# Optimization experiments

Measured on AMD Instinct MI355X. Metric: run time of the kernel, lower is better.

Reference implementation:

```python
import jax, jax.numpy as jnp
import numpy as np

R = 3
D = 2 * R + 1            # 7 displacements per axis
B, C, H, W = 2, 128, 48, 96
EPS = 1e-5


def conv2d(x, w, stride=1, padding=1):
    return jax.lax.conv_general_dilated(
        x, w, (stride, stride), [(padding, padding), (padding, padding)],
        dimension_numbers=('NCHW', 'OIHW', 'NCHW'))


def deconv2d(x, w, stride=2, padding=1):
    # w: torch ConvTranspose2d layout (I, O, kh, kw)
    wf = jnp.flip(w, (2, 3)).transpose(1, 0, 2, 3)  # -> OIHW, spatially flipped
    p = w.shape[2] - 1 - padding
    return jax.lax.conv_general_dilated(
        x, wf, (1, 1), [(p, p), (p, p)], lhs_dilation=(stride, stride),
        dimension_numbers=('NCHW', 'OIHW', 'NCHW'))


def bn_relu(x, g, b):
    # BatchNorm2d, training-mode statistics (biased variance), then ReLU
    mu = x.mean(axis=(0, 2, 3), keepdims=True)
    var = x.var(axis=(0, 2, 3), keepdims=True)
    xn = (x - mu) * jax.lax.rsqrt(var + EPS)
    return jax.nn.relu(xn * g[None, :, None, None] + b[None, :, None, None])


def grid_sample_zeros(img, gx, gy):
    # img: (B,C,H,W); gx, gy: (B,S) pixel coords. Bilinear, zero padding,
    # align_corners=True (coords already in pixel space -> identity unnormalize).
    b, c, h, w = img.shape
    x0 = jnp.floor(gx)
    y0 = jnp.floor(gy)
    wx = gx - x0
    wy = gy - y0
    imgf = img.reshape(b, c, h * w)

    def corner(xi, yi, wgt):
        valid = (xi >= 0) & (xi < w) & (yi >= 0) & (yi < h)
        xi_c = jnp.clip(xi, 0, w - 1).astype(jnp.int32)
        yi_c = jnp.clip(yi, 0, h - 1).astype(jnp.int32)
        lin = (yi_c * w + xi_c)[:, None, :]            # (B,1,S)
        v = jnp.take_along_axis(imgf, lin, axis=2)     # (B,C,S)
        return v * (wgt * valid)[:, None, :]

    return (corner(x0, y0, (1 - wx) * (1 - wy))
            + corner(x0 + 1, y0, wx * (1 - wy))
            + corner(x0, y0 + 1, (1 - wx) * wy)
            + corner(x0 + 1, y0 + 1, wx * wy))


def setup_inputs() -> dict:
    key = jax.random.key(0)
    ks = jax.random.split(key, 24)
    s = 0.05
    f1 = jax.random.normal(ks[0], (B, C, H, W), dtype=jnp.float32)
    f2 = jax.random.normal(ks[1], (B, C, H, W), dtype=jnp.float32)
    cx = jax.random.uniform(ks[2], (B, 1, H, W), dtype=jnp.float32) * (W - 1)
    cy = jax.random.uniform(ks[3], (B, 1, H, W), dtype=jnp.float32) * (H - 1)
    coords = jnp.concatenate([cx, cy], axis=1)  # (B,2,H,W): [x, y]
    p = {
        'w1': jax.random.normal(ks[4], (96, 2 * C, 3, 3)) * s,
        'g1': jnp.ones((96,)), 'b1': jnp.zeros((96,)),
        'w2': jax.random.normal(ks[5], (128, 96, 3, 3)) * s,
        'g2': jnp.ones((128,)), 'b2': jnp.zeros((128,)),
        'w3': jax.random.normal(ks[6], (128, 128, 3, 3)) * s,
        'g3': jnp.ones((128,)), 'b3': jnp.zeros((128,)),
        'w4': jax.random.normal(ks[7], (64, 128, 3, 3)) * s,
        'g4': jnp.ones((64,)), 'b4': jnp.zeros((64,)),
        'w5': jax.random.normal(ks[8], (64, 32, 4, 4)) * s,  # ConvTranspose (I,O,kh,kw)
        'g5': jnp.ones((32,)), 'b5': jnp.zeros((32,)),
        'w6': jax.random.normal(ks[9], (1, 32, 3, 3)) * s,
        'b6': jnp.zeros((1,)),
        'dap_w': jnp.eye(D * D, dtype=jnp.float32),  # identity init
    }
    return {'f1': f1, 'f2': f2, 'coords': coords, **p}


def reference(f1, f2, coords, w1, g1, b1, w2, g2, b2, w3, g3, b3,
              w4, g4, b4, w5, g5, b5, w6, b6, dap_w):
    b, c, h, w = f1.shape
    dx = jnp.linspace(-R, R, D)
    delta = jnp.stack(jnp.meshgrid(dx, dx, indexing='ij'), axis=-1)  # (D,D,2)
    cen = (coords.transpose(0, 2, 3, 1).reshape(b, 1, h, 1, w, 2)
           + delta.reshape(1, D, 1, D, 1, 2))                        # (B,D,H,D,W,2)
    gx = cen[..., 0].reshape(b, -1)
    gy = cen[..., 1].reshape(b, -1)
    f2s = grid_sample_zeros(f2, gx, gy).reshape(b, c, D, h, D, w)
    f2s = f2s.transpose(0, 2, 4, 1, 3, 5)                            # (B,D,D,C,H,W)
    f1e = jnp.broadcast_to(f1[:, None, None], (b, D, D, c, h, w))
    corr = jnp.concatenate([f1e, f2s], axis=3).reshape(b * D * D, 2 * c, h, w)
    x = bn_relu(conv2d(corr, w1), g1, b1)
    x = bn_relu(conv2d(x, w2, stride=2), g2, b2)
    x = bn_relu(conv2d(x, w3), g3, b3)
    x = bn_relu(conv2d(x, w4), g4, b4)
    x = bn_relu(deconv2d(x, w5), g5, b5)
    x = conv2d(x, w6) + b6[None, :, None, None]
    cost = x.reshape(b, D * D, h, w)
    cost = jnp.einsum('ed,bdhw->behw', dap_w, cost)  # DAP 1x1 conv, no bias
    return cost  # (B, (2r+1)^2, H, W)
```

## Files before the change

### kernel.cpp

```cpp
#include <hip/hip_runtime.h>
#include <hip/hip_bf16.h>

using bf16 = __hip_bfloat16;
typedef __attribute__((ext_vector_type(8))) short s8v;
typedef __attribute__((ext_vector_type(4))) float f4v;
typedef __attribute__((ext_vector_type(16))) float f16v;

static constexpr int Bb = 2, Hh = 48, Ww = 96;
static constexpr int HW = Hh * Ww;
static constexpr int DD = 49, Nn = Bb * DD;
static constexpr int H2 = 24, W2 = 48, HW2 = H2 * W2;

static constexpr size_t off_wf1a = 0;
static constexpr size_t off_wf1b = 221184;
static constexpr size_t off_wf3  = 442368;
static constexpr size_t off_wf2  = 737280;
static constexpr size_t off_wf4  = 958464;
static constexpr size_t off_wf5  = 1105920;
static constexpr size_t off_f1t  = 1171456;
static constexpr size_t off_y1a  = 3530752;
static constexpr size_t off_stats= 7069696;
static constexpr size_t off_f2s  = 7079936;
static constexpr size_t off_y1   = 122685440;
static constexpr size_t off_f2t  = off_y1;
static constexpr size_t off_y2   = off_f2s;
static constexpr size_t off_y3   = off_f2s + 28901376;
static constexpr size_t off_y4   = off_f2s + 57802752;
static constexpr size_t off_y5   = off_f2s + 72253440;
static constexpr size_t off_y6   = off_f2s + 101154816;
static constexpr size_t WS_NEEDED = 209389568;

__device__ __forceinline__ float bf2f(unsigned short h) {
  return __uint_as_float(((unsigned)h) << 16);
}
__device__ __forceinline__ unsigned short f2bf(float f) {
  __hip_bfloat16 h = __float2bfloat16(f);
  union { __hip_bfloat16 x; unsigned short u; } cv; cv.x = h; return cv.u;
}
template<bool EN>
__device__ __forceinline__ uint4 bn8(uint4 v, const float* a, const float* b, int c0) {
  if constexpr (!EN) return v;
  union { uint4 u; unsigned short h[8]; } X; X.u = v;
#pragma unroll
  for (int i = 0; i < 8; ++i) {
    float f = fmaxf(bf2f(X.h[i]) * a[c0 + i] + b[c0 + i], 0.f);
    X.h[i] = f2bf(f);
  }
  return X.u;
}
__device__ __forceinline__ s8v as_s8v(uint4 v) {
  union { uint4 u; s8v s; } cv; cv.u = v; return cv.s;
}

__global__ __launch_bounds__(256) void zero_k(float* __restrict__ p, int n) {
  int i = blockIdx.x * 256 + threadIdx.x;
  if (i < n) p[i] = 0.f;
}

__global__ __launch_bounds__(256) void tr_f2_k(const float* __restrict__ f2, float* __restrict__ f2t) {
  int o = blockIdx.x * 256 + threadIdx.x;
  if (o >= 2 * HW * 16) return;
  int c8 = o & 15; int pos = (o >> 4) % HW; int b = o / (HW * 16);
  float v[8];
#pragma unroll
  for (int i = 0; i < 8; ++i) v[i] = f2[((size_t)(b * 128 + c8 * 8 + i)) * HW + pos];
  float* dst = f2t + ((size_t)b * HW + pos) * 128 + c8 * 8;
#pragma unroll
  for (int i = 0; i < 8; ++i) dst[i] = v[i];
}

__global__ __launch_bounds__(256) void tr_f1_k(const float* __restrict__ f1, bf16* __restrict__ f1t) {
  int o = blockIdx.x * 256 + threadIdx.x;
  if (o >= 2 * HW * 16) return;
  int c8 = o & 15; int pos = (o >> 4) % HW; int b = o / (HW * 16);
  union { uint4 u; unsigned short h[8]; } Y;
#pragma unroll
  for (int i = 0; i < 8; ++i) Y.h[i] = f2bf(f1[((size_t)(b * 128 + c8 * 8 + i)) * HW + pos]);
  *(uint4*)(f1t + ((size_t)b * HW + pos) * 128 + c8 * 8) = Y.u;
}

__global__ __launch_bounds__(256)
void prep32_k(const float* __restrict__ w, uint4* __restrict__ wf, int NT, int CINT, int ciOff) {
  int idx = blockIdx.x * 256 + threadIdx.x;
  int total = 9 * 2 * 4 * NT * 64;
  if (idx >= total) return;
  int ocl = idx & 31; int lh = (idx >> 5) & 1;
  int q = idx >> 6; int nt = q % NT; int rest = q / NT;
  int ks = rest & 3; int cih = (rest >> 2) & 1; int khw = rest >> 3;
  int oc = nt * 32 + ocl;
  union { uint4 u; unsigned short h[8]; } Y;
#pragma unroll
  for (int i = 0; i < 8; ++i) {
    int ci = ciOff + cih * 64 + ks * 16 + lh * 8 + i;
    Y.h[i] = f2bf(w[((size_t)oc * CINT + ci) * 9 + khw]);
  }
  wf[idx] = Y.u;
}

__global__ __launch_bounds__(256)
void prep16_k(const float* __restrict__ w, uint4* __restrict__ wf, int NT, int CINT,
              int NSTAGE, int CPS, int KPS) {
  int idx = blockIdx.x * 256 + threadIdx.x;
  int total = 9 * NSTAGE * KPS * NT * 64;
  if (idx >= total) return;
  int ocl = idx & 15; int lg = (idx >> 4) & 3;
  int q = idx >> 6; int nt = q % NT; int q2 = q / NT;
  int ks = q2 % KPS; int q3 = q2 / KPS;
  int st = q3 % NSTAGE; int khw = q3 / NSTAGE;
  int oc = nt * 16 + ocl;
  union { uint4 u; unsigned short h[8]; } Y;
#pragma unroll
  for (int i = 0; i < 8; ++i) {
    int ci = st * CPS + ks * 32 + lg * 8 + i;
    Y.h[i] = f2bf(w[((size_t)oc * CINT + ci) * 9 + khw]);
  }
  wf[idx] = Y.u;
}

__global__ __launch_bounds__(256)
void prep_w5_k(const float* __restrict__ w5, uint4* __restrict__ wf) {
  int idx = blockIdx.x * 256 + threadIdx.x;
  if (idx >= 4096) return;
  int ocl = idx & 15; int lg = (idx >> 4) & 3;
  int nt = (idx >> 6) & 1; int ks = (idx >> 7) & 7; int p = idx >> 10;
  int ph = p >> 1, pw = p & 1;
  int t = ks >> 2, u = (ks >> 1) & 1;
  int kh = 3 - ph - 2 * t, kw = 3 - pw - 2 * u;
  int oc = nt * 16 + ocl;
  union { uint4 u4; unsigned short h[8]; } Y;
#pragma unroll
  for (int i = 0; i < 8; ++i) {
    int ci = (ks & 1) * 32 + lg * 8 + i;
    Y.h[i] = f2bf(w5[(((size_t)ci * 32 + oc) * 4 + kh) * 4 + kw]);
  }
  wf[idx] = Y.u4;
}

__global__ __launch_bounds__(256)
void sample_k(const float* __restrict__ f2t, const float* __restrict__ coords,
              bf16* __restrict__ f2s) {
  int wv = blockIdx.x * 4 + (threadIdx.x >> 6);
  int lane = threadIdx.x & 63;
  int p0 = wv * 32;
  for (int k = 0; k < 32; ++k) {
    int P = p0 + k;
    int hw = P % HW; int n = P / HW;
    int b = n / DD, d = n % DD;
    float gx = coords[(size_t)b * 2 * HW + hw] + (float)(d / 7 - 3);
    float gy = coords[((size_t)b * 2 + 1) * HW + hw] + (float)(d % 7 - 3);
    float x0f = floorf(gx), y0f = floorf(gy);
    float wx = gx - x0f, wy = gy - y0f;
    int x0 = (int)x0f, y0 = (int)y0f;
    const float* base = f2t + (size_t)b * HW * 128;
    float r0 = 0.f, r1 = 0.f;
#pragma unroll
    for (int c = 0; c < 4; ++c) {
      int xi = x0 + (c & 1), yi = y0 + (c >> 1);
      float wgt = ((c & 1) ? wx : 1.f - wx) * ((c >> 1) ? wy : 1.f - wy);
      if (xi < 0 || xi >= Ww || yi < 0 || yi >= Hh) wgt = 0.f;
      int xc = min(max(xi, 0), Ww - 1), yc = min(max(yi, 0), Hh - 1);
      const float* pv = base + ((size_t)(yc * Ww + xc)) * 128 + 2 * lane;
      r0 += wgt * pv[0];
      r1 += wgt * pv[1];
    }
    unsigned pack = (unsigned)f2bf(r0) | ((unsigned)f2bf(r1) << 16);
    ((unsigned*)f2s)[(size_t)P * 64 + lane] = pack;
  }
}

template<int COUT, int NT, int MT, int NB, int GR, int GC, bool OUTF32, bool HAS_BASE,
         bool HAS_BN, bool HAS_STATS>
__global__ __launch_bounds__(((GR * GC) / MT) * (NT / NB) * 64)
void conv32_k(const bf16* __restrict__ in, const uint4* __restrict__ wf,
              void* __restrict__ outv, const float* __restrict__ base,
              const float* __restrict__ bn_a, const float* __restrict__ bn_b,
              float* __restrict__ stats,
              int N, int H, int W, int DIV) {
  constexpr int NW = ((GR * GC) / MT) * (NT / NB);
  constexpr int BR = GR * 2, BC = GC * 16;
  constexpr int IR = BR + 2, IC = BC + 2;
  constexpr int INB = IR * IC * 128;
  __shared__ __align__(16) char lds[INB];

  const int tid = threadIdx.x;
  const int lane = tid & 63;
  const int wv = tid >> 6;
  const int lm = lane & 31, lh = lane >> 5;
  const int dh = lm >> 4, dw = lm & 15;
  constexpr int NG = NT / NB;
  const int mg = wv / NG, ng = wv % NG;

  const int tW = W / BC, tH = H / BR;
  const int tile = blockIdx.x % (tH * tW);
  const int n = blockIdx.x / (tH * tW);
  const int oh0 = (tile / tW) * BR, ow0 = (tile % tW) * BC;
  const size_t inbase = (size_t)n * H * W * 128;

  int trA[MT], tcA[MT];
#pragma unroll
  for (int i = 0; i < MT; ++i) { int mt = mg * MT + i; trA[i] = mt / GC; tcA[i] = mt % GC; }

  f16v acc[MT][NB];
#pragma unroll
  for (int i = 0; i < MT; ++i)
#pragma unroll
    for (int j = 0; j < NB; ++j)
#pragma unroll
      for (int r = 0; r < 16; ++r) acc[i][j][r] = 0.f;

  for (int cih = 0; cih < 2; ++cih) {
    __syncthreads();
    for (int idx = tid; idx < IR * IC * 8; idx += NW * 64) {
      int h8 = idx & 7;
      int icl = (idx >> 3) % IC;
      int ihl = (idx >> 3) / IC;
      int ih = oh0 - 1 + ihl, iw = ow0 - 1 + icl;
      uint4 v = make_uint4(0u, 0u, 0u, 0u);
      if (ih >= 0 && ih < H && iw >= 0 && iw < W) {
        v = *(const uint4*)(in + inbase + ((size_t)(ih * W + iw)) * 128 + cih * 64 + h8 * 8);
        v = bn8<HAS_BN>(v, bn_a, bn_b, cih * 64 + h8 * 8);
      }
      int bbyte = (ihl * IC + icl) * 128 + h8 * 16;
      bbyte ^= (icl & 7) << 4;
      *(uint4*)(lds + bbyte) = v;
    }
    __syncthreads();

    for (int khw = 0; khw < 9; ++khw) {
      const int kh = khw / 3, kw = khw % 3;
      const uint4* wfp = wf + (size_t)(khw * 2 + cih) * (NT * 256);
#pragma unroll
      for (int ks = 0; ks < 4; ++ks) {
        s8v Af[MT], Bf[NB];
#pragma unroll
        for (int i = 0; i < MT; ++i) {
          int rl = trA[i] * 2 + dh + kh;
          int cl = tcA[i] * 16 + dw + kw;
          int bbyte = (rl * IC + cl) * 128 + ks * 32 + lh * 16;
          bbyte ^= (cl & 7) << 4;
          Af[i] = *(const s8v*)(lds + bbyte);
        }
#pragma unroll
        for (int j = 0; j < NB; ++j)
          Bf[j] = as_s8v(wfp[(ks * NT + ng * NB + j) * 64 + lh * 32 + lm]);
#pragma unroll
        for (int i = 0; i < MT; ++i)
#pragma unroll
          for (int j = 0; j < NB; ++j)
            acc[i][j] = __builtin_amdgcn_mfma_f32_32x32x16_bf16(Af[i], Bf[j], acc[i][j], 0, 0, 0);
      }
    }
  }

  const size_t obase = (size_t)n * H * W * COUT;
  const float* bptr = nullptr;
  if constexpr (HAS_BASE) bptr = base + (size_t)(n / DIV) * H * W * COUT;

  float sacc[NB], qacc[NB];
#pragma unroll
  for (int j = 0; j < NB; ++j) { sacc[j] = 0.f; qacc[j] = 0.f; }

#pragma unroll
  for (int i = 0; i < MT; ++i) {
#pragma unroll
    for (int j = 0; j < NB; ++j) {
      int oc = (ng * NB + j) * 32 + lm;
#pragma unroll
      for (int r = 0; r < 16; ++r) {
        int row = (r & 3) + 8 * (r >> 2) + 4 * lh;
        int oh = oh0 + trA[i] * 2 + (row >> 4);
        int ow = ow0 + tcA[i] * 16 + (row & 15);
        size_t pix = (size_t)(oh * W + ow);
        float v = acc[i][j][r];
        if constexpr (HAS_BASE) v += bptr[pix * COUT + oc];
        if constexpr (HAS_STATS) { sacc[j] += v; qacc[j] += v * v; }
        if constexpr (OUTF32) ((float*)outv)[obase + pix * COUT + oc] = v;
        else ((bf16*)outv)[obase + pix * COUT + oc] = __float2bfloat16(v);
      }
    }
  }

  if constexpr (HAS_STATS) {
    __shared__ float sred[2 * COUT];
    for (int i = tid; i < 2 * COUT; i += NW * 64) sred[i] = 0.f;
    __syncthreads();
#pragma unroll
    for (int j = 0; j < NB; ++j) {
      int oc = (ng * NB + j) * 32 + lm;
      atomicAdd(&sred[oc], sacc[j]);
      atomicAdd(&sred[COUT + oc], qacc[j]);
    }
    __syncthreads();
    for (int i = tid; i < 2 * COUT; i += NW * 64) atomicAdd(&stats[i], sred[i]);
  }
}

template<int COUT, int NT, int MT, int NB, int GR, int GC, int STRIDE,
         int CINT, int CPS, int NSTAGE, int KPS, bool HAS_BN, bool HAS_STATS>
__global__ __launch_bounds__(((GR * GC) / MT) * (NT / NB) * 64)
void conv16_k(const bf16* __restrict__ in, const uint4* __restrict__ wf,
              bf16* __restrict__ out, const float* __restrict__ bn_a,
              const float* __restrict__ bn_b, float* __restrict__ stats,
              int N, int HO, int WO, int HI, int WI) {
  constexpr int NW = ((GR * GC) / MT) * (NT / NB);
  constexpr int BR = GR, BC = GC * 16;
  constexpr int IR = STRIDE * (BR - 1) + 3;
  constexpr int IC = STRIDE * (BC - 1) + 3 + (STRIDE == 2 ? 1 : 0);
  constexpr int ROWB = CPS * 2;
  constexpr int SLOTM = ROWB / 16 - 1;
  constexpr int INB = IR * IC * ROWB;
  __shared__ __align__(16) char lds[INB];

  const int tid = threadIdx.x;
  const int lane = tid & 63;
  const int wv = tid >> 6;
  const int lm = lane & 15, lg = lane >> 4;
  constexpr int NG = NT / NB;
  const int mg = wv / NG, ng = wv % NG;

  const int tW = WO / BC, tH = HO / BR;
  const int tile = blockIdx.x % (tH * tW);
  const int n = blockIdx.x / (tH * tW);
  const int oh0 = (tile / tW) * BR, ow0 = (tile % tW) * BC;
  const int ih0 = STRIDE * oh0 - 1, iw0 = STRIDE * ow0 - 1;
  const size_t inbase = (size_t)n * HI * WI * CINT;

  int trA[MT], tcA[MT];
#pragma unroll
  for (int i = 0; i < MT; ++i) { int mt = mg * MT + i; trA[i] = mt / GC; tcA[i] = mt % GC; }

  f4v acc[MT][NB];
#pragma unroll
  for (int i = 0; i < MT; ++i)
#pragma unroll
    for (int j = 0; j < NB; ++j)
#pragma unroll
      for (int r = 0; r < 4; ++r) acc[i][j][r] = 0.f;

  for (int st = 0; st < NSTAGE; ++st) {
    __syncthreads();
    for (int idx = tid; idx < IR * IC * (CPS / 8); idx += NW * 64) {
      int h8 = idx % (CPS / 8);
      int rest = idx / (CPS / 8);
      int icl = rest % IC;
      int ihl = rest / IC;
      int ih = ih0 + ihl, iw = iw0 + icl;
      uint4 v = make_uint4(0u, 0u, 0u, 0u);
      if (ih >= 0 && ih < HI && iw >= 0 && iw < WI) {
        v = *(const uint4*)(in + inbase + ((size_t)(ih * WI + iw)) * CINT + st * CPS + h8 * 8);
        v = bn8<HAS_BN>(v, bn_a, bn_b, st * CPS + h8 * 8);
      }
      int bbyte = (ihl * IC + icl) * ROWB + h8 * 16;
      bbyte ^= ((icl >> (STRIDE - 1)) & SLOTM) << 4;
      *(uint4*)(lds + bbyte) = v;
    }
    __syncthreads();

    for (int khw = 0; khw < 9; ++khw) {
      const int kh = khw / 3, kw = khw % 3;
      const uint4* wfp = wf + (size_t)(khw * NSTAGE + st) * (KPS * NT * 64);
#pragma unroll
      for (int ks = 0; ks < KPS; ++ks) {
        s8v Af[MT], Bf[NB];
#pragma unroll
        for (int i = 0; i < MT; ++i) {
          int rl = STRIDE * trA[i] + kh;
          int cl = STRIDE * (tcA[i] * 16 + lm) + kw;
          int bbyte = (rl * IC + cl) * ROWB + ks * 64 + lg * 16;
          bbyte ^= ((cl >> (STRIDE - 1)) & SLOTM) << 4;
          Af[i] = *(const s8v*)(lds + bbyte);
        }
#pragma unroll
        for (int j = 0; j < NB; ++j)
          Bf[j] = as_s8v(wfp[(ks * NT + ng * NB + j) * 64 + lg * 16 + lm]);
#pragma unroll
        for (int i = 0; i < MT; ++i)
#pragma unroll
          for (int j = 0; j < NB; ++j)
            acc[i][j] = __builtin_amdgcn_mfma_f32_16x16x32_bf16(Af[i], Bf[j], acc[i][j], 0, 0, 0);
      }
    }
  }

  const size_t obase = (size_t)n * HO * WO * COUT;
  float sacc[NB], qacc[NB];
#pragma unroll
  for (int j = 0; j < NB; ++j) { sacc[j] = 0.f; qacc[j] = 0.f; }

#pragma unroll
  for (int i = 0; i < MT; ++i) {
#pragma unroll
    for (int j = 0; j < NB; ++j) {
      int oc = (ng * NB + j) * 16 + lm;
#pragma unroll
      for (int r = 0; r < 4; ++r) {
        int oh = oh0 + trA[i];
        int ow = ow0 + tcA[i] * 16 + lg * 4 + r;
        float v = acc[i][j][r];
        if constexpr (HAS_STATS) { sacc[j] += v; qacc[j] += v * v; }
        out[obase + (size_t)(oh * WO + ow) * COUT + oc] = __float2bfloat16(v);
      }
    }
  }

  if constexpr (HAS_STATS) {
    __shared__ float sred[2 * COUT];
    for (int i = tid; i < 2 * COUT; i += NW * 64) sred[i] = 0.f;
    __syncthreads();
#pragma unroll
    for (int j = 0; j < NB; ++j) {
      int oc = (ng * NB + j) * 16 + lm;
      atomicAdd(&sred[oc], sacc[j]);
      atomicAdd(&sred[COUT + oc], qacc[j]);
    }
    __syncthreads();
    for (int i = tid; i < 2 * COUT; i += NW * 64) atomicAdd(&stats[i], sred[i]);
  }
}

__global__ __launch_bounds__(256)
void deconv16_k(const bf16* __restrict__ in, const uint4* __restrict__ wf5,
                bf16* __restrict__ out, const float* __restrict__ a4,
                const float* __restrict__ b4, float* __restrict__ stats) {
  constexpr int IR = 6, IC = 50, INB = IR * IC * 128;
  __shared__ __align__(16) char lds[INB];
  __shared__ float sred[64];
  const int tid = threadIdx.x;
  const int lane = tid & 63, wv = tid >> 6;
  const int lm = lane & 15, lg = lane >> 4;
  const int n = blockIdx.x / 6;
  const int qh0 = (blockIdx.x % 6) * 4;
  const size_t ibase = (size_t)n * HW2 * 64;

  for (int idx = tid; idx < 64; idx += 256) sred[idx] = 0.f;

  for (int idx = tid; idx < IR * IC * 8; idx += 256) {
    int h8 = idx & 7; int icl = (idx >> 3) % IC; int ihl = (idx >> 3) / IC;
    int ih = qh0 - 1 + ihl, iw = -1 + icl;
    uint4 v = make_uint4(0u, 0u, 0u, 0u);
    if (ih >= 0 && ih < H2 && iw >= 0 && iw < W2) {
      v = *(const uint4*)(in + ibase + ((size_t)(ih * W2 + iw)) * 64 + h8 * 8);
      v = bn8<true>(v, a4, b4, h8 * 8);
    }
    int bbyte = (ihl * IC + icl) * 128 + h8 * 16;
    bbyte ^= (icl & 7) << 4;
    *(uint4*)(lds + bbyte) = v;
  }
  __syncthreads();

  int trA[3], tcA[3];
#pragma unroll
  for (int i = 0; i < 3; ++i) { int mt = wv * 3 + i; trA[i] = mt / 3; tcA[i] = mt % 3; }

  float sacc[2], qacc[2];
  sacc[0] = sacc[1] = qacc[0] = qacc[1] = 0.f;

  for (int p = 0; p < 4; ++p) {
    const int ph = p >> 1, pw = p & 1;
    f4v acc[3][2];
#pragma unroll
    for (int i = 0; i < 3; ++i)
#pragma unroll
      for (int j = 0; j < 2; ++j)
#pragma unroll
        for (int r = 0; r < 4; ++r) acc[i][j][r] = 0.f;
#pragma unroll
    for (int ks = 0; ks < 8; ++ks) {
      int t = ks >> 2, u = (ks >> 1) & 1, cb = ks & 1;
      s8v Af[3], Bf[2];
#pragma unroll
      for (int i = 0; i < 3; ++i) {
        int rl = trA[i] + t + ph;
        int cl = tcA[i] * 16 + lm + u + pw;
        int bbyte = (rl * IC + cl) * 128 + cb * 64 + lg * 16;
        bbyte ^= (cl & 7) << 4;
        Af[i] = *(const s8v*)(lds + bbyte);
      }
#pragma unroll
      for (int j = 0; j < 2; ++j)
        Bf[j] = as_s8v(wf5[p * 1024 + (ks * 2 + j) * 64 + lg * 16 + lm]);
#pragma unroll
      for (int i = 0; i < 3; ++i)
#pragma unroll
        for (int j = 0; j < 2; ++j)
          acc[i][j] = __builtin_amdgcn_mfma_f32_16x16x32_bf16(Af[i], Bf[j], acc[i][j], 0, 0, 0);
    }
#pragma unroll
    for (int i = 0; i < 3; ++i) {
#pragma unroll
      for (int j = 0; j < 2; ++j) {
        int oc = j * 16 + lm;
#pragma unroll
        for (int r = 0; r < 4; ++r) {
          int qh = qh0 + trA[i];
          int qw = tcA[i] * 16 + lg * 4 + r;
          int oh = 2 * qh + ph, ow = 2 * qw + pw;
          float v = acc[i][j][r];
          sacc[j] += v; qacc[j] += v * v;
          out[((size_t)n * HW + oh * Ww + ow) * 32 + oc] = __float2bfloat16(v);
        }
      }
    }
  }

  __syncthreads();
#pragma unroll
  for (int j = 0; j < 2; ++j) {
    int oc = j * 16 + lm;
    atomicAdd(&sred[oc], sacc[j]);
    atomicAdd(&sred[32 + oc], qacc[j]);
  }
  __syncthreads();
  for (int i = tid; i < 64; i += 256) atomicAdd(&stats[i], sred[i]);
}

__global__ void bnfin_k(const float* __restrict__ sums, const float* __restrict__ gamma,
                        const float* __restrict__ beta, float* __restrict__ ab, int C, float invCnt) {
  int c = blockIdx.x * blockDim.x + threadIdx.x;
  if (c >= C) return;
  float mean = sums[c] * invCnt;
  float var = sums[C + c] * invCnt - mean * mean;
  float a = gamma[c] * rsqrtf(var + 1e-5f);
  ab[c] = a;
  ab[C + c] = beta[c] - mean * a;
}

__global__ __launch_bounds__(256)
void conv6_k(const bf16* __restrict__ y5, const float* __restrict__ w6,
             const float* __restrict__ b6, const float* __restrict__ a5,
             const float* __restrict__ bb5, float* __restrict__ y6) {
  int o = blockIdx.x * 256 + threadIdx.x;
  if (o >= Nn * HW) return;
  int hw = o % HW; int n = o / HW;
  int h = hw / Ww, w = hw % Ww;
  float acc = b6[0];
  for (int kh = 0; kh < 3; ++kh) {
    int ih = h - 1 + kh; if (ih < 0 || ih >= Hh) continue;
    for (int kw = 0; kw < 3; ++kw) {
      int iw = w - 1 + kw; if (iw < 0 || iw >= Ww) continue;
      const bf16* p = y5 + ((size_t)n * HW + ih * Ww + iw) * 32;
      int khw = kh * 3 + kw;
#pragma unroll
      for (int c8 = 0; c8 < 4; ++c8) {
        union { uint4 u; unsigned short hh[8]; } X;
        X.u = *(const uint4*)(p + c8 * 8);
#pragma unroll
        for (int i = 0; i < 8; ++i) {
          int c = c8 * 8 + i;
          float f = fmaxf(bf2f(X.hh[i]) * a5[c] + bb5[c], 0.f);
          acc += f * w6[c * 9 + khw];
        }
      }
    }
  }
  y6[o] = acc;
}

__global__ __launch_bounds__(256)
void dap_k(const float* __restrict__ y6, const float* __restrict__ dap, float* __restrict__ out) {
  int o = blockIdx.x * 256 + threadIdx.x;
  if (o >= Bb * DD * HW) return;
  int hw = o % HW;
  int e = (o / HW) % DD;
  int b = o / (HW * DD);
  float s = 0.f;
#pragma unroll 7
  for (int d = 0; d < DD; ++d) s += dap[e * DD + d] * y6[((size_t)(b * DD + d)) * HW + hw];
  out[o] = s;
}

extern "C" void kernel_launch(void* const* d_in, const int* in_sizes, int n_in,
                              void* d_out, int out_size, void* d_ws, size_t ws_size,
                              hipStream_t stream) {
  const float* f1 = (const float*)d_in[0];
  const float* f2 = (const float*)d_in[1];
  const float* coords = (const float*)d_in[2];
  const float* w1 = (const float*)d_in[3];
  const float* g1 = (const float*)d_in[4];
  const float* b1 = (const float*)d_in[5];
  const float* w2 = (const float*)d_in[6];
  const float* g2 = (const float*)d_in[7];
  const float* b2 = (const float*)d_in[8];
  const float* w3 = (const float*)d_in[9];
  const float* g3 = (const float*)d_in[10];
  const float* b3 = (const float*)d_in[11];
  const float* w4 = (const float*)d_in[12];
  const float* g4 = (const float*)d_in[13];
  const float* b4 = (const float*)d_in[14];
  const float* w5 = (const float*)d_in[15];
  const float* g5 = (const float*)d_in[16];
  const float* b5 = (const float*)d_in[17];
  const float* w6 = (const float*)d_in[18];
  const float* b6 = (const float*)d_in[19];
  const float* dap = (const float*)d_in[20];
  float* out = (float*)d_out;
  char* ws = (char*)d_ws;
  if (ws_size < WS_NEEDED) return;

  uint4* wf1a = (uint4*)(ws + off_wf1a);
  uint4* wf1b = (uint4*)(ws + off_wf1b);
  uint4* wf3 = (uint4*)(ws + off_wf3);
  uint4* wf2 = (uint4*)(ws + off_wf2);
  uint4* wf4 = (uint4*)(ws + off_wf4);
  uint4* wf5 = (uint4*)(ws + off_wf5);
  bf16* f1t = (bf16*)(ws + off_f1t);
  float* y1a = (float*)(ws + off_y1a);
  float* f2t = (float*)(ws + off_f2t);
  bf16* f2s = (bf16*)(ws + off_f2s);
  bf16* y1 = (bf16*)(ws + off_y1);
  bf16* y2 = (bf16*)(ws + off_y2);
  bf16* y3 = (bf16*)(ws + off_y3);
  bf16* y4 = (bf16*)(ws + off_y4);
  bf16* y5 = (bf16*)(ws + off_y5);
  float* y6 = (float*)(ws + off_y6);
  float* st0 = (float*)(ws + off_stats) + 0 * 512;
  float* st1 = (float*)(ws + off_stats) + 1 * 512;
  float* st2 = (float*)(ws + off_stats) + 2 * 512;
  float* st3 = (float*)(ws + off_stats) + 3 * 512;
  float* st4 = (float*)(ws + off_stats) + 4 * 512;

  zero_k<<<10, 256, 0, stream>>>((float*)(ws + off_stats), 2560);

  tr_f2_k<<<576, 256, 0, stream>>>(f2, f2t);
  tr_f1_k<<<576, 256, 0, stream>>>(f1, f1t);
  prep32_k<<<54, 256, 0, stream>>>(w1, wf1a, 3, 256, 0);
  prep32_k<<<54, 256, 0, stream>>>(w1, wf1b, 3, 256, 128);
  prep32_k<<<72, 256, 0, stream>>>(w3, wf3, 4, 128, 0);
  prep16_k<<<54, 256, 0, stream>>>(w2, wf2, 8, 96, 3, 32, 1);
  prep16_k<<<36, 256, 0, stream>>>(w4, wf4, 4, 128, 2, 64, 2);
  prep_w5_k<<<16, 256, 0, stream>>>(w5, wf5);

  sample_k<<<3528, 256, 0, stream>>>(f2t, coords, f2s);

  conv32_k<96, 3, 2, 3, 4, 2, true, false, false, false><<<36, 256, 0, stream>>>(
      f1t, wf1a, y1a, nullptr, nullptr, nullptr, nullptr, 2, Hh, Ww, 1);
  conv32_k<96, 3, 2, 3, 4, 2, false, true, false, true><<<1764, 256, 0, stream>>>(
      f2s, wf1b, y1, y1a, nullptr, nullptr, st0, Nn, Hh, Ww, DD);
  bnfin_k<<<1, 256, 0, stream>>>(st0, g1, b1, st0 + 256, 96, 1.f / (98.f * 4608.f));

  conv16_k<128, 8, 3, 4, 2, 3, 2, 96, 32, 3, 1, true, true><<<1176, 256, 0, stream>>>(
      y1, wf2, y2, st0 + 256, st0 + 256 + 96, st1, Nn, H2, W2, Hh, Ww);
  bnfin_k<<<1, 256, 0, stream>>>(st1, g2, b2, st1 + 256, 128, 1.f / (98.f * 1152.f));

  conv32_k<128, 4, 3, 2, 2, 3, false, false, true, true><<<588, 256, 0, stream>>>(
      y2, wf3, y3, nullptr, st1 + 256, st1 + 256 + 128, st2, Nn, H2, W2, 1);
  bnfin_k<<<1, 256, 0, stream>>>(st2, g3, b3, st2 + 256, 128, 1.f / (98.f * 1152.f));

  conv16_k<64, 4, 3, 4, 4, 3, 1, 128, 64, 2, 2, true, true><<<588, 256, 0, stream>>>(
      y3, wf4, y4, st2 + 256, st2 + 256 + 128, st3, Nn, H2, W2, H2, W2);
  bnfin_k<<<1, 256, 0, stream>>>(st3, g4, b4, st3 + 256, 64, 1.f / (98.f * 1152.f));

  deconv16_k<<<588, 256, 0, stream>>>(y4, wf5, y5, st3 + 256, st3 + 256 + 64, st4);
  bnfin_k<<<1, 256, 0, stream>>>(st4, g5, b5, st4 + 256, 32, 1.f / (98.f * 4608.f));

  conv6_k<<<1764, 256, 0, stream>>>(y5, w6, b6, st4 + 256, st4 + 256 + 32, y6);

  dap_k<<<1764, 256, 0, stream>>>(y6, dap, out);
}
```

Measured before the change: 767.1 us.

## Software-pipeline conv input staging in 32-channel slices with register prefetch

The conv32 and conv16 kernels now stage input tiles into LDS in 32-channel slices instead of 64/128-channel chunks. Each block prefetches the next slice into registers while running MFMAs on the current one, then commits it to LDS between two barriers. This shrinks LDS per block, which can raise occupancy, and is meant to hide global-load latency behind the matrix math. It also introduces a new XOR swizzle for the narrower LDS rows, changes the weight-prep layout for conv4 to match, and costs more barriers plus extra staging registers.

```diff
diff --git a/kernel.cpp b/kernel.cpp
--- a/kernel.cpp
+++ b/kernel.cpp
@@ -51,6 +51,7 @@
 __device__ __forceinline__ s8v as_s8v(uint4 v) {
   union { uint4 u; s8v s; } cv; cv.u = v; return cv.s;
 }
+__device__ __forceinline__ int swz(int icl) { return ((icl >> 1) ^ (icl >> 3)) & 3; }
 
 __global__ __launch_bounds__(256) void zero_k(float* __restrict__ p, int n) {
   int i = blockIdx.x * 256 + threadIdx.x;
@@ -168,19 +169,60 @@
   }
 }
 
-template<int COUT, int NT, int MT, int NB, int GR, int GC, bool OUTF32, bool HAS_BASE,
-         bool HAS_BN, bool HAS_STATS>
+template<int NLD, int NTHR, int NGRAN, int IC, int CIN>
+__device__ __forceinline__ void stage_issue(const bf16* __restrict__ in, size_t inbase,
+    int ih0, int iw0, int HI, int WI, int ksl, int tid, uint4 (&stg)[NLD]) {
+#pragma unroll
+  for (int t = 0; t < NLD; ++t) {
+    int idx = tid + t * NTHR;
+    uint4 v = make_uint4(0u, 0u, 0u, 0u);
+    if (idx < NGRAN) {
+      int h8 = idx & 3; int pix = idx >> 2;
+      int icl = pix % IC, ihl = pix / IC;
+      int ih = ih0 + ihl, iw = iw0 + icl;
+      if (ih >= 0 && ih < HI && iw >= 0 && iw < WI)
+        v = *(const uint4*)(in + inbase + ((size_t)(ih * WI + iw)) * CIN + ksl * 32 + h8 * 8);
+    }
+    stg[t] = v;
+  }
+}
+
+template<int NLD, int NTHR, int NGRAN, int IC, int ROWB, bool HAS_BN>
+__device__ __forceinline__ void stage_commit(char* __restrict__ lds,
+    const float* __restrict__ a, const float* __restrict__ b,
+    int ih0, int iw0, int HI, int WI, int ksl, int tid, uint4 (&stg)[NLD]) {
+#pragma unroll
+  for (int t = 0; t < NLD; ++t) {
+    int idx = tid + t * NTHR;
+    if (idx < NGRAN) {
+      int h8 = idx & 3; int pix = idx >> 2;
+      int icl = pix % IC, ihl = pix / IC;
+      uint4 v = stg[t];
+      if constexpr (HAS_BN) {
+        int ih = ih0 + ihl, iw = iw0 + icl;
+        if (ih >= 0 && ih < HI && iw >= 0 && iw < WI) v = bn8<true>(v, a, b, ksl * 32 + h8 * 8);
+      }
+      int g = h8 ^ swz(icl);
+      *(uint4*)(lds + (ihl * IC + icl) * ROWB + g * 16) = v;
+    }
+  }
+}
+
+template<int COUT, int NT, int MT, int NB, int GR, int GC, int CIN,
+         bool OUTF32, bool HAS_BASE, bool HAS_BN, bool HAS_STATS>
 __global__ __launch_bounds__(((GR * GC) / MT) * (NT / NB) * 64)
 void conv32_k(const bf16* __restrict__ in, const uint4* __restrict__ wf,
               void* __restrict__ outv, const float* __restrict__ base,
               const float* __restrict__ bn_a, const float* __restrict__ bn_b,
-              float* __restrict__ stats,
-              int N, int H, int W, int DIV) {
+              float* __restrict__ stats, int N, int H, int W, int DIV) {
   constexpr int NW = ((GR * GC) / MT) * (NT / NB);
+  constexpr int NTHR = NW * 64;
   constexpr int BR = GR * 2, BC = GC * 16;
   constexpr int IR = BR + 2, IC = BC + 2;
-  constexpr int INB = IR * IC * 128;
-  __shared__ __align__(16) char lds[INB];
+  constexpr int NSL = CIN / 32;
+  constexpr int NGRAN = IR * IC * 4;
+  constexpr int NLD = (NGRAN + NTHR - 1) / NTHR;
+  __shared__ __align__(16) char lds[IR * IC * 64];
 
   const int tid = threadIdx.x;
   const int lane = tid & 63;
@@ -194,7 +236,8 @@
   const int tile = blockIdx.x % (tH * tW);
   const int n = blockIdx.x / (tH * tW);
   const int oh0 = (tile / tW) * BR, ow0 = (tile % tW) * BC;
-  const size_t inbase = (size_t)n * H * W * 128;
+  const int ih0 = oh0 - 1, iw0 = ow0 - 1;
+  const size_t inbase = (size_t)n * H * W * CIN;
 
   int trA[MT], tcA[MT];
 #pragma unroll
@@ -208,47 +251,49 @@
 #pragma unroll
       for (int r = 0; r < 16; ++r) acc[i][j][r] = 0.f;
 
-  for (int cih = 0; cih < 2; ++cih) {
-    __syncthreads();
-    for (int idx = tid; idx < IR * IC * 8; idx += NW * 64) {
-      int h8 = idx & 7;
-      int icl = (idx >> 3) % IC;
-      int ihl = (idx >> 3) / IC;
-      int ih = oh0 - 1 + ihl, iw = ow0 - 1 + icl;
-      uint4 v = make_uint4(0u, 0u, 0u, 0u);
-      if (ih >= 0 && ih < H && iw >= 0 && iw < W) {
-        v = *(const uint4*)(in + inbase + ((size_t)(ih * W + iw)) * 128 + cih * 64 + h8 * 8);
-        v = bn8<HAS_BN>(v, bn_a, bn_b, cih * 64 + h8 * 8);
-      }
-      int bbyte = (ihl * IC + icl) * 128 + h8 * 16;
-      bbyte ^= (icl & 7) << 4;
-      *(uint4*)(lds + bbyte) = v;
-    }
-    __syncthreads();
-
+  {
+    uint4 stg0[NLD];
+    stage_issue<NLD, NTHR, NGRAN, IC, CIN>(in, inbase, ih0, iw0, H, W, 0, tid, stg0);
+    stage_commit<NLD, NTHR, NGRAN, IC, 64, HAS_BN>(lds, bn_a, bn_b, ih0, iw0, H, W, 0, tid, stg0);
+  }
+  __syncthreads();
+
+#pragma unroll
+  for (int ksl = 0; ksl < NSL; ++ksl) {
+    uint4 stgN[NLD];
+    if (ksl + 1 < NSL)
+      stage_issue<NLD, NTHR, NGRAN, IC, CIN>(in, inbase, ih0, iw0, H, W, ksl + 1, tid, stgN);
+
+#pragma unroll
     for (int khw = 0; khw < 9; ++khw) {
       const int kh = khw / 3, kw = khw % 3;
-      const uint4* wfp = wf + (size_t)(khw * 2 + cih) * (NT * 256);
-#pragma unroll
-      for (int ks = 0; ks < 4; ++ks) {
+      const uint4* wfp = wf + (size_t)(khw * 2 + (ksl >> 1)) * (NT * 256);
+#pragma unroll
+      for (int ks = 0; ks < 2; ++ks) {
         s8v Af[MT], Bf[NB];
 #pragma unroll
         for (int i = 0; i < MT; ++i) {
           int rl = trA[i] * 2 + dh + kh;
           int cl = tcA[i] * 16 + dw + kw;
-          int bbyte = (rl * IC + cl) * 128 + ks * 32 + lh * 16;
-          bbyte ^= (cl & 7) << 4;
-          Af[i] = *(const s8v*)(lds + bbyte);
+          int g = (ks * 2 + lh) ^ swz(cl);
+          Af[i] = *(const s8v*)(lds + (rl * IC + cl) * 64 + g * 16);
         }
+        int ks4 = (ksl & 1) * 2 + ks;
 #pragma unroll
         for (int j = 0; j < NB; ++j)
-          Bf[j] = as_s8v(wfp[(ks * NT + ng * NB + j) * 64 + lh * 32 + lm]);
+          Bf[j] = as_s8v(wfp[(ks4 * NT + ng * NB + j) * 64 + lane]);
 #pragma unroll
         for (int i = 0; i < MT; ++i)
 #pragma unroll
           for (int j = 0; j < NB; ++j)
             acc[i][j] = __builtin_amdgcn_mfma_f32_32x32x16_bf16(Af[i], Bf[j], acc[i][j], 0, 0, 0);
       }
+    }
+
+    if (ksl + 1 < NSL) {
+      __syncthreads();
+      stage_commit<NLD, NTHR, NGRAN, IC, 64, HAS_BN>(lds, bn_a, bn_b, ih0, iw0, H, W, ksl + 1, tid, stgN);
+      __syncthreads();
     }
   }
 
@@ -282,7 +327,7 @@
 
   if constexpr (HAS_STATS) {
     __shared__ float sred[2 * COUT];
-    for (int i = tid; i < 2 * COUT; i += NW * 64) sred[i] = 0.f;
+    for (int i = tid; i < 2 * COUT; i += NTHR) sred[i] = 0.f;
     __syncthreads();
 #pragma unroll
     for (int j = 0; j < NB; ++j) {
@@ -291,25 +336,27 @@
       atomicAdd(&sred[COUT + oc], qacc[j]);
     }
     __syncthreads();
-    for (int i = tid; i < 2 * COUT; i += NW * 64) atomicAdd(&stats[i], sred[i]);
+    for (int i = tid; i < 2 * COUT; i += NTHR) atomicAdd(&stats[i], sred[i]);
   }
 }
 
 template<int COUT, int NT, int MT, int NB, int GR, int GC, int STRIDE,
-         int CINT, int CPS, int NSTAGE, int KPS, bool HAS_BN, bool HAS_STATS>
+         int CINT, bool HAS_BN, bool HAS_STATS>
 __global__ __launch_bounds__(((GR * GC) / MT) * (NT / NB) * 64)
 void conv16_k(const bf16* __restrict__ in, const uint4* __restrict__ wf,
               bf16* __restrict__ out, const float* __restrict__ bn_a,
               const float* __restrict__ bn_b, float* __restrict__ stats,
               int N, int HO, int WO, int HI, int WI) {
   constexpr int NW = ((GR * GC) / MT) * (NT / NB);
+  constexpr int NTHR = NW * 64;
   constexpr int BR = GR, BC = GC * 16;
   constexpr int IR = STRIDE * (BR - 1) + 3;
   constexpr int IC = STRIDE * (BC - 1) + 3 + (STRIDE == 2 ? 1 : 0);
-  constexpr int ROWB = CPS * 2;
-  constexpr int SLOTM = ROWB / 16 - 1;
-  constexpr int INB = IR * IC * ROWB;
-  __shared__ __align__(16) char lds[INB];
+  constexpr int ROWB = (STRIDE == 2) ? 80 : 64;
+  constexpr int NSL = CINT / 32;
+  constexpr int NGRAN = IR * IC * 4;
+  constexpr int NLD = (NGRAN + NTHR - 1) / NTHR;
+  __shared__ __align__(16) char lds[IR * IC * ROWB];
 
   const int tid = threadIdx.x;
   const int lane = tid & 63;
@@ -337,48 +384,45 @@
 #pragma unroll
       for (int r = 0; r < 4; ++r) acc[i][j][r] = 0.f;
 
-  for (int st = 0; st < NSTAGE; ++st) {
-    __syncthreads();
-    for (int idx = tid; idx < IR * IC * (CPS / 8); idx += NW * 64) {
-      int h8 = idx % (CPS / 8);
-      int rest = idx / (CPS / 8);
-      int icl = rest % IC;
-      int ihl = rest / IC;
-      int ih = ih0 + ihl, iw = iw0 + icl;
-      uint4 v = make_uint4(0u, 0u, 0u, 0u);
-      if (ih >= 0 && ih < HI && iw >= 0 && iw < WI) {
-        v = *(const uint4*)(in + inbase + ((size_t)(ih * WI + iw)) * CINT + st * CPS + h8 * 8);
-        v = bn8<HAS_BN>(v, bn_a, bn_b, st * CPS + h8 * 8);
-      }
-      int bbyte = (ihl * IC + icl) * ROWB + h8 * 16;
-      bbyte ^= ((icl >> (STRIDE - 1)) & SLOTM) << 4;
-      *(uint4*)(lds + bbyte) = v;
-    }
-    __syncthreads();
-
+  {
+    uint4 stg0[NLD];
+    stage_issue<NLD, NTHR, NGRAN, IC, CINT>(in, inbase, ih0, iw0, HI, WI, 0, tid, stg0);
+    stage_commit<NLD, NTHR, NGRAN, IC, ROWB, HAS_BN>(lds, bn_a, bn_b, ih0, iw0, HI, WI, 0, tid, stg0);
+  }
+  __syncthreads();
+
+#pragma unroll
+  for (int ksl = 0; ksl < NSL; ++ksl) {
+    uint4 stgN[NLD];
+    if (ksl + 1 < NSL)
+      stage_issue<NLD, NTHR, NGRAN, IC, CINT>(in, inbase, ih0, iw0, HI, WI, ksl + 1, tid, stgN);
+
+#pragma unroll
     for (int khw = 0; khw < 9; ++khw) {
       const int kh = khw / 3, kw = khw % 3;
-      const uint4* wfp = wf + (size_t)(khw * NSTAGE + st) * (KPS * NT * 64);
-#pragma unroll
-      for (int ks = 0; ks < KPS; ++ks) {
-        s8v Af[MT], Bf[NB];
-#pragma unroll
-        for (int i = 0; i < MT; ++i) {
-          int rl = STRIDE * trA[i] + kh;
-          int cl = STRIDE * (tcA[i] * 16 + lm) + kw;
-          int bbyte = (rl * IC + cl) * ROWB + ks * 64 + lg * 16;
-          bbyte ^= ((cl >> (STRIDE - 1)) & SLOTM) << 4;
-          Af[i] = *(const s8v*)(lds + bbyte);
-        }
+      const uint4* wfp = wf + (size_t)(khw * NSL + ksl) * (NT * 64);
+      s8v Af[MT], Bf[NB];
+#pragma unroll
+      for (int i = 0; i < MT; ++i) {
+        int rl = STRIDE * trA[i] + kh;
+        int cl = STRIDE * (tcA[i] * 16 + lm) + kw;
+        int g = lg ^ swz(cl);
+        Af[i] = *(const s8v*)(lds + (rl * IC + cl) * ROWB + g * 16);
+      }
+#pragma unroll
+      for (int j = 0; j < NB; ++j)
+        Bf[j] = as_s8v(wfp[(ng * NB + j) * 64 + lane]);
+#pragma unroll
+      for (int i = 0; i < MT; ++i)
 #pragma unroll
         for (int j = 0; j < NB; ++j)
-          Bf[j] = as_s8v(wfp[(ks * NT + ng * NB + j) * 64 + lg * 16 + lm]);
-#pragma unroll
-        for (int i = 0; i < MT; ++i)
-#pragma unroll
-          for (int j = 0; j < NB; ++j)
-            acc[i][j] = __builtin_amdgcn_mfma_f32_16x16x32_bf16(Af[i], Bf[j], acc[i][j], 0, 0, 0);
-      }
+          acc[i][j] = __builtin_amdgcn_mfma_f32_16x16x32_bf16(Af[i], Bf[j], acc[i][j], 0, 0, 0);
+    }
+
+    if (ksl + 1 < NSL) {
+      __syncthreads();
+      stage_commit<NLD, NTHR, NGRAN, IC, ROWB, HAS_BN>(lds, bn_a, bn_b, ih0, iw0, HI, WI, ksl + 1, tid, stgN);
+      __syncthreads();
     }
   }
 
@@ -405,7 +449,7 @@
 
   if constexpr (HAS_STATS) {
     __shared__ float sred[2 * COUT];
-    for (int i = tid; i < 2 * COUT; i += NW * 64) sred[i] = 0.f;
+    for (int i = tid; i < 2 * COUT; i += NTHR) sred[i] = 0.f;
     __syncthreads();
 #pragma unroll
     for (int j = 0; j < NB; ++j) {
@@ -414,7 +458,7 @@
       atomicAdd(&sred[COUT + oc], qacc[j]);
     }
     __syncthreads();
-    for (int i = tid; i < 2 * COUT; i += NW * 64) atomicAdd(&stats[i], sred[i]);
+    for (int i = tid; i < 2 * COUT; i += NTHR) atomicAdd(&stats[i], sred[i]);
   }
 }
 
@@ -627,26 +671,26 @@
   prep32_k<<<54, 256, 0, stream>>>(w1, wf1b, 3, 256, 128);
   prep32_k<<<72, 256, 0, stream>>>(w3, wf3, 4, 128, 0);
   prep16_k<<<54, 256, 0, stream>>>(w2, wf2, 8, 96, 3, 32, 1);
-  prep16_k<<<36, 256, 0, stream>>>(w4, wf4, 4, 128, 2, 64, 2);
+  prep16_k<<<36, 256, 0, stream>>>(w4, wf4, 4, 128, 4, 32, 1);
   prep_w5_k<<<16, 256, 0, stream>>>(w5, wf5);
 
   sample_k<<<3528, 256, 0, stream>>>(f2t, coords, f2s);
 
-  conv32_k<96, 3, 2, 3, 4, 2, true, false, false, false><<<36, 256, 0, stream>>>(
+  conv32_k<96, 3, 2, 3, 4, 2, 128, true, false, false, false><<<36, 256, 0, stream>>>(
       f1t, wf1a, y1a, nullptr, nullptr, nullptr, nullptr, 2, Hh, Ww, 1);
-  conv32_k<96, 3, 2, 3, 4, 2, false, true, false, true><<<1764, 256, 0, stream>>>(
+  conv32_k<96, 3, 2, 3, 4, 2, 128, false, true, false, true><<<1764, 256, 0, stream>>>(
       f2s, wf1b, y1, y1a, nullptr, nullptr, st0, Nn, Hh, Ww, DD);
   bnfin_k<<<1, 256, 0, stream>>>(st0, g1, b1, st0 + 256, 96, 1.f / (98.f * 4608.f));
 
-  conv16_k<128, 8, 3, 4, 2, 3, 2, 96, 32, 3, 1, true, true><<<1176, 256, 0, stream>>>(
+  conv16_k<128, 8, 3, 4, 2, 3, 2, 96, true, true><<<1176, 256, 0, stream>>>(
       y1, wf2, y2, st0 + 256, st0 + 256 + 96, st1, Nn, H2, W2, Hh, Ww);
   bnfin_k<<<1, 256, 0, stream>>>(st1, g2, b2, st1 + 256, 128, 1.f / (98.f * 1152.f));
 
-  conv32_k<128, 4, 3, 2, 2, 3, false, false, true, true><<<588, 256, 0, stream>>>(
+  conv32_k<128, 4, 3, 2, 2, 3, 128, false, false, true, true><<<588, 256, 0, stream>>>(
       y2, wf3, y3, nullptr, st1 + 256, st1 + 256 + 128, st2, Nn, H2, W2, 1);
   bnfin_k<<<1, 256, 0, stream>>>(st2, g3, b3, st2 + 256, 128, 1.f / (98.f * 1152.f));
 
-  conv16_k<64, 4, 3, 4, 4, 3, 1, 128, 64, 2, 2, true, true><<<588, 256, 0, stream>>>(
+  conv16_k<64, 4, 3, 4, 4, 3, 1, 128, true, true><<<588, 256, 0, stream>>>(
       y3, wf4, y4, st2 + 256, st2 + 256 + 128, st3, Nn, H2, W2, H2, W2);
   bnfin_k<<<1, 256, 0, stream>>>(st3, g4, b4, st3 + 256, 64, 1.f / (98.f * 1152.f));
 
```

Measured after the change: 686.5 us. 1.12x faster.
